# Performance work log

Measured on AMD Instinct MI355X. Metric: run time of the kernel, lower is better.

## Reference

```python
import jax, jax.numpy as jnp
import numpy as np

B, T, C = 2, 2048, 768
NH = 12
HS = C // NH


def setup_inputs() -> dict:
    key = jax.random.key(0)
    k1, k2, k3 = jax.random.split(key, 3)
    x = jax.random.normal(k1, (B, T, C), dtype=jnp.float32)
    # c_attn: Linear(C, 3C). Stored as (C, 3C) so y = x @ w + b (same math as torch x @ W.T + b).
    w_attn = jax.random.normal(k2, (C, 3 * C), dtype=jnp.float32) * (1.0 / np.sqrt(C))
    b_attn = jax.random.normal(k3, (3 * C,), dtype=jnp.float32) * 0.02
    return {"x": x, "w_attn": w_attn, "b_attn": b_attn}


def reference(x, w_attn, b_attn):
    b, t, c = x.shape
    qkv = x @ w_attn + b_attn                      # [B, T, 3C]
    q, k, v = jnp.split(qkv, 3, axis=-1)
    # [B, T, C] -> [B, NH, T, HS]
    q = q.reshape(b, t, NH, HS).transpose(0, 2, 1, 3)
    k = k.reshape(b, t, NH, HS).transpose(0, 2, 1, 3)
    v = v.reshape(b, t, NH, HS).transpose(0, 2, 1, 3)
    scale = 1.0 / np.sqrt(HS).astype(np.float32)
    wei = jnp.einsum("bhqd,bhkd->bhqk", q, k) * scale   # [B, NH, T, T]
    causal = jnp.tril(jnp.ones((t, t), dtype=bool))
    wei = jnp.where(causal[None, None, :, :], wei, -jnp.inf)
    wei = jax.nn.softmax(wei, axis=-1)
    out = jnp.einsum("bhqk,bhkd->bhqd", wei, v)          # [B, NH, T, HS]
    # NOTE: original module returns here, before head-merge / output projection.
    return out
```

## Files before the change

### kernel.cpp

```cpp
#include <hip/hip_runtime.h>

typedef __bf16 bf16_t;
typedef __bf16 bf16x8 __attribute__((ext_vector_type(8)));
typedef __bf16 bf16x4 __attribute__((ext_vector_type(4)));
typedef _Float16 f16x2 __attribute__((ext_vector_type(2)));
typedef _Float16 f16x4 __attribute__((ext_vector_type(4)));
typedef _Float16 f16x8 __attribute__((ext_vector_type(8)));
typedef float f32x4 __attribute__((ext_vector_type(4)));

#define B_   2
#define T_   2048
#define C_   768
#define NH_  12
#define HS_  64
#define N3_  2304
#define M_   4096
#define QSCALE 0.18033688011112042f

__device__ __forceinline__ bf16_t f2bf(float f) {
  unsigned u = __builtin_bit_cast(unsigned, f);
  u += 0x7fffu + ((u >> 16) & 1u);
  unsigned short s = (unsigned short)(u >> 16);
  return __builtin_bit_cast(bf16_t, s);
}

__global__ __launch_bounds__(256) void cvt_xw_kernel(const float* __restrict__ x,
                                                     const float* __restrict__ w,
                                                     bf16_t* __restrict__ xb,
                                                     bf16_t* __restrict__ wt) {
  __shared__ float tile[32][33];
  int bx = blockIdx.x;
  if (bx < 3072) {
    int i = (bx * 256 + threadIdx.x) * 4;
    float4 v = *reinterpret_cast<const float4*>(x + i);
    xb[i + 0] = f2bf(v.x);
    xb[i + 1] = f2bf(v.y);
    xb[i + 2] = f2bf(v.z);
    xb[i + 3] = f2bf(v.w);
  } else {
    int b = bx - 3072;
    int k0 = (b % 24) * 32, n0 = (b / 24) * 32;
    int tx = threadIdx.x & 31, ty = threadIdx.x >> 5;
#pragma unroll
    for (int i = 0; i < 4; i++)
      tile[ty + i * 8][tx] = w[(size_t)(k0 + ty + i * 8) * N3_ + n0 + tx];
    __syncthreads();
#pragma unroll
    for (int i = 0; i < 4; i++)
      wt[(size_t)(n0 + ty + i * 8) * C_ + k0 + tx] = f2bf(tile[tx][ty + i * 8]);
  }
}

__global__ __launch_bounds__(256) void gemm_qkv(const bf16_t* __restrict__ xb,
                                                const bf16_t* __restrict__ wt,
                                                const float* __restrict__ bias,
                                                bf16_t* __restrict__ qout,
                                                bf16_t* __restrict__ kout,
                                                _Float16* __restrict__ va) {
  __shared__ bf16_t As[2][128 * 32];
  __shared__ bf16_t Bs[2][128 * 32];
  const int tid = threadIdx.x;
  const int lane = tid & 63, wave = tid >> 6;
  const int wm = wave >> 1, wn = wave & 1;
  const int quad = lane >> 4, l15 = lane & 15;
  const int row0 = blockIdx.y * 128;
  const int col0 = blockIdx.x * 128;
  const bool isqk = (col0 < 1536);

  f32x4 acc[4][4];
#pragma unroll
  for (int mi = 0; mi < 4; mi++)
#pragma unroll
    for (int ni = 0; ni < 4; ni++) acc[mi][ni] = f32x4{0.f, 0.f, 0.f, 0.f};

  for (int k0 = 0; k0 < C_; k0 += 64) {
#pragma unroll
    for (int h = 0; h < 2; h++) {
#pragma unroll
      for (int c = 0; c < 2; c++) {
        int chunk = c * 256 + tid;
        int r = chunk >> 2, qd = chunk & 3;
        const bf16_t* ga = xb + (size_t)(row0 + r) * C_ + k0 + h * 32 + qd * 8;
        const bf16_t* gb = wt + (size_t)(col0 + r) * C_ + k0 + h * 32 + qd * 8;
        char* la = (char*)As[h] + (size_t)(c * 256 + wave * 64) * 16;
        char* lb = (char*)Bs[h] + (size_t)(c * 256 + wave * 64) * 16;
        __builtin_amdgcn_global_load_lds((const __attribute__((address_space(1))) void*)ga,
                                         (__attribute__((address_space(3))) void*)la, 16, 0, 0);
        __builtin_amdgcn_global_load_lds((const __attribute__((address_space(1))) void*)gb,
                                         (__attribute__((address_space(3))) void*)lb, 16, 0, 0);
      }
    }
    __syncthreads();

    bf16x8 af[4][2], bfr[4][2];
#pragma unroll
    for (int mi = 0; mi < 4; mi++)
#pragma unroll
      for (int h = 0; h < 2; h++)
        af[mi][h] = *reinterpret_cast<const bf16x8*>(&As[h][(wm * 64 + mi * 16 + l15) * 32 + quad * 8]);
#pragma unroll
    for (int ni = 0; ni < 4; ni++)
#pragma unroll
      for (int h = 0; h < 2; h++)
        bfr[ni][h] = *reinterpret_cast<const bf16x8*>(&Bs[h][(wn * 64 + ni * 16 + l15) * 32 + quad * 8]);
    if (isqk) {
#pragma unroll
      for (int h = 0; h < 2; h++)
#pragma unroll
        for (int mi = 0; mi < 4; mi++)
#pragma unroll
          for (int ni = 0; ni < 4; ni++)
            acc[mi][ni] = __builtin_amdgcn_mfma_f32_16x16x32_bf16(bfr[ni][h], af[mi][h], acc[mi][ni], 0, 0, 0);
    } else {
#pragma unroll
      for (int h = 0; h < 2; h++)
#pragma unroll
        for (int mi = 0; mi < 4; mi++)
#pragma unroll
          for (int ni = 0; ni < 4; ni++)
            acc[mi][ni] = __builtin_amdgcn_mfma_f32_16x16x32_bf16(af[mi][h], bfr[ni][h], acc[mi][ni], 0, 0, 0);
    }
    __syncthreads();
  }

  if (isqk) {
#pragma unroll
    for (int mi = 0; mi < 4; mi++) {
      int t = row0 + wm * 64 + mi * 16 + l15;
      int b = t >> 11, tt = t & 2047;
#pragma unroll
      for (int ni = 0; ni < 4; ni++) {
        int cN0 = col0 + wn * 64 + ni * 16 + quad * 4;
        int which = cN0 / 768;
        int rem = cN0 - which * 768;
        int h = rem >> 6, d0 = rem & 63;
        float4 bv = *reinterpret_cast<const float4*>(bias + cN0);
        float sc = which ? 1.0f : QSCALE;
        bf16x4 pack;
        pack[0] = f2bf((acc[mi][ni][0] + bv.x) * sc);
        pack[1] = f2bf((acc[mi][ni][1] + bv.y) * sc);
        pack[2] = f2bf((acc[mi][ni][2] + bv.z) * sc);
        pack[3] = f2bf((acc[mi][ni][3] + bv.w) * sc);
        bf16_t* dst = which ? kout : qout;
        *reinterpret_cast<bf16x4*>(dst + (((size_t)b * NH_ + h) * T_ + tt) * HS_ + d0) = pack;
      }
    }
  } else {
#pragma unroll
    for (int mi = 0; mi < 4; mi++) {
      int trow = row0 + wm * 64 + mi * 16 + quad * 4;
      int b = trow >> 11, tt = trow & 2047;
      int kt = tt >> 6, nj = (tt >> 4) & 3, qd = (tt >> 2) & 3;
#pragma unroll
      for (int ni = 0; ni < 4; ni++) {
        int cN = col0 + wn * 64 + ni * 16 + l15;
        int rem = cN - 1536;
        int h = rem >> 6, d = rem & 63;
        int bh = b * NH_ + h;
        float bv = bias[cN];
        f16x4 pk;
#pragma unroll
        for (int r = 0; r < 4; r++) pk[r] = (_Float16)(acc[mi][ni][r] + bv);
        size_t off = ((((((size_t)bh * 32 + kt) * 4 + nj) * 4 + qd) * 16 + (d & 15)) * 16) + (d >> 4) * 4;
        *reinterpret_cast<f16x4*>(va + off) = pk;
      }
    }
  }
}

__global__ __launch_bounds__(256) void attn_kernel(const bf16_t* __restrict__ qb,
                                                   const bf16_t* __restrict__ kb,
                                                   const _Float16* __restrict__ va,
                                                   float* __restrict__ out) {
  __shared__ bf16_t Ks[2][64][72];
  __shared__ _Float16 Vs[2][4][2][64][8];
  const int tid = threadIdx.x;
  const int lane = tid & 63, wave = tid >> 6;
  const int quad = lane >> 4, l15 = lane & 15;
  const int pairIdx = (int)blockIdx.x;
  const int bh = (int)blockIdx.z * NH_ + (int)blockIdx.y;
  const bf16_t* Qg = qb + (size_t)bh * T_ * HS_;
  const bf16_t* Kg = kb + (size_t)bh * T_ * HS_;
  const _Float16* Vg = va + (size_t)bh * 32 * 4096;

  const int krow = tid >> 2, kcol = (tid & 3) * 16;
  const int vni = tid >> 6, vlane = tid & 63;

  int4 rk0, rk1, rv0, rv1;
  const char* kp;
  const char* vp;
  auto GLOAD = [&]() {
    rk0 = *reinterpret_cast<const int4*>(kp);
    rk1 = *reinterpret_cast<const int4*>(kp + 16);
    rv0 = *reinterpret_cast<const int4*>(vp);
    rv1 = *reinterpret_cast<const int4*>(vp + 16);
    kp += 8192; vp += 8192;
  };
  auto SSTORE = [&](int buf) {
    char* kd = (char*)&Ks[buf][krow][kcol];
    *reinterpret_cast<int4*>(kd) = rk0;
    *reinterpret_cast<int4*>(kd + 16) = rk1;
    *reinterpret_cast<int4*>(&Vs[buf][vni][0][vlane][0]) = rv0;
    *reinterpret_cast<int4*>(&Vs[buf][vni][1][vlane][0]) = rv1;
  };

#pragma unroll
  for (int part = 0; part < 2; part++) {
    const int qtile = part ? pairIdx : 31 - pairIdx;
    const int qrow_base = qtile * 64 + wave * 16;
    const int qmax = qrow_base + 15;
    const int qcol = qrow_base + l15;
    const int nkt = qtile + 1;

    bf16x8 bq0 = *reinterpret_cast<const bf16x8*>(Qg + (size_t)qcol * HS_ + quad * 8);
    bf16x8 bq1 = *reinterpret_cast<const bf16x8*>(Qg + (size_t)qcol * HS_ + 32 + quad * 8);

    float lsum = 0.f;
    f32x4 Oacc[4];
#pragma unroll
    for (int mi = 0; mi < 4; mi++) Oacc[mi] = f32x4{0.f, 0.f, 0.f, 0.f};

    kp = (const char*)Kg + krow * 128 + kcol * 2;
    vp = (const char*)Vg + tid * 32;
    GLOAD();
    __syncthreads();
    SSTORE(0);
    __syncthreads();

    for (int kt = 0; kt < nkt; kt++) {
      const int cur = kt & 1;
      const bool last = (kt + 1 >= nkt);
      if (!last) GLOAD();

      const bool diag = (kt == nkt - 1);
      f16x4 pf[4];
#pragma unroll
      for (int ni = 0; ni < 4; ni++) {
        if (diag && (kt * 64 + ni * 16 > qmax)) continue;
        bf16x8 ka0 = *reinterpret_cast<const bf16x8*>(&Ks[cur][ni * 16 + l15][quad * 8]);
        bf16x8 ka1 = *reinterpret_cast<const bf16x8*>(&Ks[cur][ni * 16 + l15][32 + quad * 8]);
        f32x4 s = {0.f, 0.f, 0.f, 0.f};
        s = __builtin_amdgcn_mfma_f32_16x16x32_bf16(ka0, bq0, s, 0, 0, 0);
        s = __builtin_amdgcn_mfma_f32_16x16x32_bf16(ka1, bq1, s, 0, 0, 0);
        float p0 = __builtin_amdgcn_exp2f(s[0]);
        float p1 = __builtin_amdgcn_exp2f(s[1]);
        float p2 = __builtin_amdgcn_exp2f(s[2]);
        float p3 = __builtin_amdgcn_exp2f(s[3]);
        if (diag) {
          int jb = kt * 64 + ni * 16 + quad * 4;
          if (jb + 0 > qcol) p0 = 0.f;
          if (jb + 1 > qcol) p1 = 0.f;
          if (jb + 2 > qcol) p2 = 0.f;
          if (jb + 3 > qcol) p3 = 0.f;
        }
        lsum += (p0 + p1) + (p2 + p3);
        f16x2 lo2 = __builtin_bit_cast(f16x2, __builtin_amdgcn_cvt_pkrtz(p0, p1));
        f16x2 hi2 = __builtin_bit_cast(f16x2, __builtin_amdgcn_cvt_pkrtz(p2, p3));
        pf[ni] = f16x4{lo2[0], lo2[1], hi2[0], hi2[1]};
      }
#pragma unroll
      for (int ni = 0; ni < 4; ni++) {
        if (diag && (kt * 64 + ni * 16 > qmax)) continue;
#pragma unroll
        for (int p = 0; p < 2; p++) {
          f16x8 vv = *reinterpret_cast<const f16x8*>(&Vs[cur][ni][p][lane][0]);
          f16x4 lo = __builtin_shufflevector(vv, vv, 0, 1, 2, 3);
          f16x4 hi = __builtin_shufflevector(vv, vv, 4, 5, 6, 7);
          Oacc[2 * p]     = __builtin_amdgcn_mfma_f32_16x16x16f16(lo, pf[ni], Oacc[2 * p], 0, 0, 0);
          Oacc[2 * p + 1] = __builtin_amdgcn_mfma_f32_16x16x16f16(hi, pf[ni], Oacc[2 * p + 1], 0, 0, 0);
        }
      }

      if (!last) {
        SSTORE(1 - cur);
        __syncthreads();
      }
    }

    lsum += __shfl_xor(lsum, 16, 64);
    lsum += __shfl_xor(lsum, 32, 64);
    float rinv = 1.0f / lsum;

#pragma unroll
    for (int mi = 0; mi < 4; mi++) {
      float4 o;
      o.x = Oacc[mi][0] * rinv;
      o.y = Oacc[mi][1] * rinv;
      o.z = Oacc[mi][2] * rinv;
      o.w = Oacc[mi][3] * rinv;
      *reinterpret_cast<float4*>(out + ((size_t)bh * T_ + qcol) * HS_ + mi * 16 + quad * 4) = o;
    }
  }
}

extern "C" void kernel_launch(void* const* d_in, const int* in_sizes, int n_in,
                              void* d_out, int out_size, void* d_ws, size_t ws_size,
                              hipStream_t stream) {
  const float* x = (const float*)d_in[0];
  const float* w = (const float*)d_in[1];
  const float* bias = (const float*)d_in[2];
  float* out = (float*)d_out;

  char* ws = (char*)d_ws;
  bf16_t* xb = (bf16_t*)(ws);
  bf16_t* wt = (bf16_t*)(ws + 6291456);
  bf16_t* qb = (bf16_t*)(ws + 6291456 + 3538944);
  bf16_t* kb = qb + 3145728;
  _Float16* va = (_Float16*)(kb + 3145728);

  cvt_xw_kernel<<<dim3(3072 + 1728), dim3(256), 0, stream>>>(x, w, xb, wt);
  gemm_qkv<<<dim3(N3_ / 128, M_ / 128), dim3(256), 0, stream>>>(xb, wt, bias, qb, kb, va);
  attn_kernel<<<dim3(16, NH_, B_), dim3(256), 0, stream>>>(qb, kb, va, out);
}
```

Baseline: 146.2 us.

## Double-buffer QKV GEMM LDS tiles to overlap global loads with MFMA

Restructures the QKV projection GEMM main loop from a single-stage 64-wide K step into a 32-wide K step with two LDS buffers. The next tile is prefetched with global_load_lds while MFMAs consume the current one, and global pointers are precomputed outside the loop. The aim is to hide global-memory latency behind compute. In exchange the loop has twice as many iterations and barriers, and correctness depends on the single barrier per iteration ordering the async LDS writes against the reads.

```diff
diff --git a/kernel.cpp b/kernel.cpp
--- a/kernel.cpp
+++ b/kernel.cpp
@@ -73,52 +73,54 @@
 #pragma unroll
     for (int ni = 0; ni < 4; ni++) acc[mi][ni] = f32x4{0.f, 0.f, 0.f, 0.f};
 
-  for (int k0 = 0; k0 < C_; k0 += 64) {
-#pragma unroll
-    for (int h = 0; h < 2; h++) {
-#pragma unroll
-      for (int c = 0; c < 2; c++) {
-        int chunk = c * 256 + tid;
-        int r = chunk >> 2, qd = chunk & 3;
-        const bf16_t* ga = xb + (size_t)(row0 + r) * C_ + k0 + h * 32 + qd * 8;
-        const bf16_t* gb = wt + (size_t)(col0 + r) * C_ + k0 + h * 32 + qd * 8;
-        char* la = (char*)As[h] + (size_t)(c * 256 + wave * 64) * 16;
-        char* lb = (char*)Bs[h] + (size_t)(c * 256 + wave * 64) * 16;
-        __builtin_amdgcn_global_load_lds((const __attribute__((address_space(1))) void*)ga,
-                                         (__attribute__((address_space(3))) void*)la, 16, 0, 0);
-        __builtin_amdgcn_global_load_lds((const __attribute__((address_space(1))) void*)gb,
-                                         (__attribute__((address_space(3))) void*)lb, 16, 0, 0);
-      }
-    }
-    __syncthreads();
-
-    bf16x8 af[4][2], bfr[4][2];
+  const int r0 = tid >> 2, q0 = tid & 3;
+  const int r1 = (256 + tid) >> 2, q1 = (256 + tid) & 3;
+  const bf16_t* gA0 = xb + (size_t)(row0 + r0) * C_ + q0 * 8;
+  const bf16_t* gA1 = xb + (size_t)(row0 + r1) * C_ + q1 * 8;
+  const bf16_t* gB0 = wt + (size_t)(col0 + r0) * C_ + q0 * 8;
+  const bf16_t* gB1 = wt + (size_t)(col0 + r1) * C_ + q1 * 8;
+  const int ldsOff0 = (wave * 64) * 16;
+  const int ldsOff1 = (256 + wave * 64) * 16;
+
+  auto STAGE = [&](int buf, int k0) {
+    __builtin_amdgcn_global_load_lds((const __attribute__((address_space(1))) void*)(gA0 + k0),
+                                     (__attribute__((address_space(3))) void*)((char*)As[buf] + ldsOff0), 16, 0, 0);
+    __builtin_amdgcn_global_load_lds((const __attribute__((address_space(1))) void*)(gA1 + k0),
+                                     (__attribute__((address_space(3))) void*)((char*)As[buf] + ldsOff1), 16, 0, 0);
+    __builtin_amdgcn_global_load_lds((const __attribute__((address_space(1))) void*)(gB0 + k0),
+                                     (__attribute__((address_space(3))) void*)((char*)Bs[buf] + ldsOff0), 16, 0, 0);
+    __builtin_amdgcn_global_load_lds((const __attribute__((address_space(1))) void*)(gB1 + k0),
+                                     (__attribute__((address_space(3))) void*)((char*)Bs[buf] + ldsOff1), 16, 0, 0);
+  };
+
+  STAGE(0, 0);
+  __syncthreads();
+
+  constexpr int NT = C_ / 32;
+#pragma unroll 2
+  for (int t = 0; t < NT; ++t) {
+    const int cur = t & 1;
+    if (t + 1 < NT) STAGE(cur ^ 1, (t + 1) * 32);
+
+    bf16x8 af[4], bfr[4];
 #pragma unroll
     for (int mi = 0; mi < 4; mi++)
-#pragma unroll
-      for (int h = 0; h < 2; h++)
-        af[mi][h] = *reinterpret_cast<const bf16x8*>(&As[h][(wm * 64 + mi * 16 + l15) * 32 + quad * 8]);
+      af[mi] = *reinterpret_cast<const bf16x8*>(&As[cur][(wm * 64 + mi * 16 + l15) * 32 + quad * 8]);
 #pragma unroll
     for (int ni = 0; ni < 4; ni++)
-#pragma unroll
-      for (int h = 0; h < 2; h++)
-        bfr[ni][h] = *reinterpret_cast<const bf16x8*>(&Bs[h][(wn * 64 + ni * 16 + l15) * 32 + quad * 8]);
+      bfr[ni] = *reinterpret_cast<const bf16x8*>(&Bs[cur][(wn * 64 + ni * 16 + l15) * 32 + quad * 8]);
     if (isqk) {
 #pragma unroll
-      for (int h = 0; h < 2; h++)
-#pragma unroll
-        for (int mi = 0; mi < 4; mi++)
-#pragma unroll
-          for (int ni = 0; ni < 4; ni++)
-            acc[mi][ni] = __builtin_amdgcn_mfma_f32_16x16x32_bf16(bfr[ni][h], af[mi][h], acc[mi][ni], 0, 0, 0);
+      for (int mi = 0; mi < 4; mi++)
+#pragma unroll
+        for (int ni = 0; ni < 4; ni++)
+          acc[mi][ni] = __builtin_amdgcn_mfma_f32_16x16x32_bf16(bfr[ni], af[mi], acc[mi][ni], 0, 0, 0);
     } else {
 #pragma unroll
-      for (int h = 0; h < 2; h++)
-#pragma unroll
-        for (int mi = 0; mi < 4; mi++)
-#pragma unroll
-          for (int ni = 0; ni < 4; ni++)
-            acc[mi][ni] = __builtin_amdgcn_mfma_f32_16x16x32_bf16(af[mi][h], bfr[ni][h], acc[mi][ni], 0, 0, 0);
+      for (int mi = 0; mi < 4; mi++)
+#pragma unroll
+        for (int ni = 0; ni < 4; ni++)
+          acc[mi][ni] = __builtin_amdgcn_mfma_f32_16x16x32_bf16(af[mi], bfr[ni], acc[mi][ni], 0, 0, 0);
     }
     __syncthreads();
   }
```

After: 147.0 us. About the same (+0.5%).
